# Optimization experiments

Hardware: AMD Instinct MI355X
Metric: run time of the kernel (lower is better)

Reference implementation:

```python
import jax, jax.numpy as jnp
import numpy as np

A = 2048        # atoms
IN_DEPTH = 128
OUT_DEPTH = 128
FILTER_LEN = 16


def setup_inputs() -> dict:
    key = jax.random.key(0)
    k1, k2, k3, k4 = jax.random.split(key, 4)
    node_property_tensor = jax.random.normal(k1, (A, IN_DEPTH), dtype=jnp.float32)
    connectivity_tensor = jax.random.normal(k2, (A, A, FILTER_LEN), dtype=jnp.float32)
    bond_property_tensor = jax.random.normal(k3, (A, FILTER_LEN, 2), dtype=jnp.float32)
    # filters initialized ~ N(0,1) * 1/in_depth, per the torch init
    filters = jax.random.normal(k4, (OUT_DEPTH, FILTER_LEN, IN_DEPTH + 2), dtype=jnp.float32) / IN_DEPTH
    return {
        "node_property_tensor": node_property_tensor,
        "connectivity_tensor": connectivity_tensor,
        "bond_property_tensor": bond_property_tensor,
        "filters": filters,
    }


def reference(node_property_tensor, connectivity_tensor, bond_property_tensor, filters):
    # gather neighbor features: conn (A,B,F) x node (B,D) -> (A,F,D)
    node_connection = jnp.einsum('abf,bd->afd', connectivity_tensor, node_property_tensor)
    # append bond properties -> (A, F, D+2)
    combined = jnp.concatenate([node_connection, bond_property_tensor], axis=2)
    # fused broadcast-multiply + double-sum: (A,F,K) x (O,F,K) -> (A,O)
    return jnp.einsum('afk,ofk->ao', combined, filters)
```

## Files before the change

### kernel.cpp

```cpp
#include <hip/hip_runtime.h>
#include <stdint.h>

#define N_ATOM 2048
#define K_TOT  32768
#define KCH    2048
#define BK2    128
#define NIT    (KCH / BK2)

typedef __attribute__((ext_vector_type(8))) short bf16x8;
typedef __attribute__((ext_vector_type(4))) float f32x4;

typedef __attribute__((address_space(3))) uint32_t lds_u32;
typedef __attribute__((address_space(1))) uint32_t gbl_u32;

__device__ __forceinline__ void async_ld16(const void* g, void* l) {
  __builtin_amdgcn_global_load_lds((const gbl_u32*)g, (lds_u32*)l, 16, 0, 0);
}

__device__ __forceinline__ unsigned short f2bf(float x) {
  union { float f; uint32_t u; } v; v.f = x;
  uint32_t r = v.u + 0x7FFFu + ((v.u >> 16) & 1u);
  return (unsigned short)(r >> 16);
}

__device__ __forceinline__ uint32_t pack_bf2(float x, float y) {
  union { float f; uint32_t u; } a, b;
  a.f = x; b.f = y;
  uint32_t au = a.u + 0x7FFFu;
  uint32_t bu = b.u + 0x7FFFu;
  return __builtin_amdgcn_perm(bu, au, 0x07060302u);
}

__global__ __launch_bounds__(256) void k_pre(const float* __restrict__ node,
                                             const float* __restrict__ filt,
                                             const float* __restrict__ bond,
                                             unsigned short* __restrict__ Gt,
                                             float* __restrict__ out) {
  __shared__ unsigned short SM[2 * 128 * 136];
  const int t   = threadIdx.x;
  const int bid = blockIdx.x;

  if (bid < 256) {
    unsigned short* As = SM;
    unsigned short* Bs = SM + 128 * 136;
    const int b0 = (bid & 15) * 128;
    const int n0 = (bid >> 4) * 128;

#pragma unroll
    for (int rep = 0; rep < 16; ++rep) {
      int q = rep * 256 + t;
      int row = q >> 5, c4 = q & 31;
      float4 v = *(const float4*)(node + (size_t)(b0 + row) * 128 + c4 * 4);
      unsigned short* dst = &As[row * 136 + c4 * 4];
      dst[0] = f2bf(v.x); dst[1] = f2bf(v.y); dst[2] = f2bf(v.z); dst[3] = f2bf(v.w);
    }
#pragma unroll
    for (int rep = 0; rep < 32; ++rep) {
      int q = rep * 256 + t;
      int row = q >> 6, c2 = q & 63;
      float2 v = *(const float2*)(filt + (size_t)(n0 + row) * 130 + c2 * 2);
      unsigned short* dst = &Bs[row * 136 + c2 * 2];
      dst[0] = f2bf(v.x); dst[1] = f2bf(v.y);
    }
    __syncthreads();

    const int w = t >> 6, l = t & 63;
    const int lm = l & 15, q4 = l >> 4;

    f32x4 acc[2][8];
#pragma unroll
    for (int ms = 0; ms < 2; ++ms)
#pragma unroll
      for (int ns = 0; ns < 8; ++ns)
        acc[ms][ns] = (f32x4){0.f, 0.f, 0.f, 0.f};

#pragma unroll
    for (int ks = 0; ks < 4; ++ks) {
      int ko = ks * 32 + q4 * 8;
      bf16x8 a[2], b[8];
#pragma unroll
      for (int ms = 0; ms < 2; ++ms) {
        int m = w * 32 + ms * 16 + lm;
        a[ms] = *(const bf16x8*)&As[m * 136 + ko];
      }
#pragma unroll
      for (int ns = 0; ns < 8; ++ns) {
        int n = ns * 16 + lm;
        b[ns] = *(const bf16x8*)&Bs[n * 136 + ko];
      }
#pragma unroll
      for (int ms = 0; ms < 2; ++ms)
#pragma unroll
        for (int ns = 0; ns < 8; ++ns)
          acc[ms][ns] = __builtin_amdgcn_mfma_f32_16x16x32_bf16(a[ms], b[ns], acc[ms][ns], 0, 0, 0);
    }

#pragma unroll
    for (int ms = 0; ms < 2; ++ms)
#pragma unroll
      for (int ns = 0; ns < 8; ++ns)
#pragma unroll
        for (int i = 0; i < 4; ++i) {
          int m = w * 32 + ms * 16 + q4 * 4 + i;
          int n = ns * 16 + lm;
          Gt[(size_t)(b0 + m) * 2048 + n0 + n] = f2bf(acc[ms][ns][i]);
        }
  } else {
    float* fb = (float*)SM;
    float* bl = (float*)SM + 128 * 32;
    const int a0 = (bid - 256) * 16;

#pragma unroll
    for (int r = 0; r < 16; ++r) {
      int idx = r * 256 + t;
      int o = idx >> 5, fj = idx & 31;
      int f = fj >> 1, j = fj & 1;
      fb[idx] = filt[(size_t)o * 2080 + f * 130 + 128 + j];
    }
    bl[t]       = bond[(size_t)a0 * 32 + t];
    bl[256 + t] = bond[(size_t)a0 * 32 + 256 + t];
    __syncthreads();

#pragma unroll
    for (int r = 0; r < 8; ++r) {
      int idx = r * 256 + t;
      int aa = idx >> 7, o = idx & 127;
      const float2* bp = (const float2*)&bl[aa * 32];
      const float2* fp = (const float2*)&fb[o * 32];
      float acc = 0.f;
#pragma unroll
      for (int f = 0; f < 16; ++f) {
        float2 b2 = bp[f], f2 = fp[f];
        acc += b2.x * f2.x + b2.y * f2.y;
      }
      out[(size_t)(a0 + aa) * 128 + o] = acc;
    }
  }
}

__global__ __launch_bounds__(256, 2) void k_main(const float* __restrict__ conn,
                                                 const unsigned short* __restrict__ Gt,
                                                 float* __restrict__ out) {
  __shared__ unsigned short Bh[2][8 * 128 * 16];

  const int t  = threadIdx.x;
  const int w  = t >> 6, l = t & 63;
  const int lm = l & 15, q4 = l >> 4;
  const int a0 = blockIdx.x * 64;
  const int kc = blockIdx.y * KCH;

  f32x4 acc[8];
#pragma unroll
  for (int ns = 0; ns < 8; ++ns)
    acc[ns] = (f32x4){0.f, 0.f, 0.f, 0.f};

  const float* arow = conn + (size_t)(a0 + w * 16 + lm) * K_TOT;

  auto stageB = [&](int buf, int k0) {
    const char* gB = (const char*)(Gt + (size_t)k0 * 128);
#pragma unroll
    for (int r = 0; r < 8; ++r) {
      const void* g = gB + (size_t)(r * 256 + t) * 16;
      void* lb = (void*)((char*)&Bh[buf][0] + r * 4096 + w * 1024);
      async_ld16(g, lb);
    }
  };

  f32x4 Ar[2][4][2];
#define LOADA(BUF, K0)                                                      \
  do {                                                                      \
    _Pragma("unroll") for (int kk = 0; kk < 4; ++kk) {                      \
      const float* p = arow + (K0) + kk * 32 + q4 * 8;                      \
      Ar[BUF][kk][0] = __builtin_nontemporal_load((const f32x4*)p);         \
      Ar[BUF][kk][1] = __builtin_nontemporal_load((const f32x4*)(p + 4));   \
    }                                                                       \
  } while (0)

  stageB(0, kc);
  LOADA(0, kc);
  LOADA(1, kc + BK2);
  __builtin_amdgcn_sched_barrier(0);
  asm volatile("s_waitcnt vmcnt(16)" ::: "memory");
  __builtin_amdgcn_s_barrier();
  __builtin_amdgcn_sched_barrier(0);

#pragma unroll
  for (int it = 0; it < NIT; ++it) {
    const int cur = it & 1;

    if (it + 1 < NIT) stageB(1 - cur, kc + (it + 1) * BK2);

    bf16x8 af[4];
#pragma unroll
    for (int kk = 0; kk < 4; ++kk) {
      f32x4 lo = Ar[cur][kk][0], hi = Ar[cur][kk][1];
      union { bf16x8 v; uint32_t u[4]; } cvt;
      cvt.u[0] = pack_bf2(lo[0], lo[1]);
      cvt.u[1] = pack_bf2(lo[2], lo[3]);
      cvt.u[2] = pack_bf2(hi[0], hi[1]);
      cvt.u[3] = pack_bf2(hi[2], hi[3]);
      af[kk] = cvt.v;
    }

    if (it + 2 < NIT) LOADA(cur, kc + (it + 2) * BK2);

#pragma unroll
    for (int kk = 0; kk < 4; ++kk) {
      const int b_rel = 2 * kk + (q4 >> 1);
      const int f0 = (q4 & 1) * 8;
#pragma unroll
      for (int ns = 0; ns < 8; ++ns) {
        int o = ns * 16 + lm;
        bf16x8 b = *(const bf16x8*)&Bh[cur][b_rel * 2048 + o * 16 + f0];
        acc[ns] = __builtin_amdgcn_mfma_f32_16x16x32_bf16(af[kk], b, acc[ns], 0, 0, 0);
      }
    }

    if (it + 1 < NIT) {
      __builtin_amdgcn_sched_barrier(0);
      if (it + 2 < NIT) {
        asm volatile("s_waitcnt vmcnt(8)" ::: "memory");
      } else {
        asm volatile("s_waitcnt vmcnt(0)" ::: "memory");
      }
      __builtin_amdgcn_s_barrier();
      __builtin_amdgcn_sched_barrier(0);
    }
  }
#undef LOADA

#pragma unroll
  for (int ns = 0; ns < 8; ++ns)
#pragma unroll
    for (int i = 0; i < 4; ++i) {
      int m = w * 16 + q4 * 4 + i;
      int n = ns * 16 + lm;
      atomicAdd(&out[(size_t)(a0 + m) * 128 + n], acc[ns][i]);
    }
}

extern "C" void kernel_launch(void* const* d_in, const int* in_sizes, int n_in,
                              void* d_out, int out_size, void* d_ws, size_t ws_size,
                              hipStream_t stream) {
  const float* node = (const float*)d_in[0];
  const float* conn = (const float*)d_in[1];
  const float* bond = (const float*)d_in[2];
  const float* filt = (const float*)d_in[3];
  float* out = (float*)d_out;

  if (ws_size < (size_t)N_ATOM * 2048 * sizeof(unsigned short)) return;
  unsigned short* Gt = (unsigned short*)d_ws;

  k_pre <<<dim3(384),    256, 0, stream>>>(node, filt, bond, Gt, out);
  k_main<<<dim3(32, 16), 256, 0, stream>>>(conn, Gt, out);
}
```

Baseline: 407.5 us.

## Read B operand directly from global memory instead of staging through LDS

Removes the LDS double buffer for the bf16 Gt operand in the main kernel, along with its async global-to-LDS loads, waitcnt fences and workgroup barriers. Each wave now loads its B fragments straight from global memory (expected to hit L2/L1) right before the MFMAs. This drops the barrier synchronisation and frees shared memory, which may raise occupancy. In exchange, every wave issues redundant global loads of the same B tile, and those loads now sit on the MFMA critical path with no explicit prefetch.

```diff
diff --git a/kernel.cpp b/kernel.cpp
--- a/kernel.cpp
+++ b/kernel.cpp
@@ -9,13 +9,6 @@
 
 typedef __attribute__((ext_vector_type(8))) short bf16x8;
 typedef __attribute__((ext_vector_type(4))) float f32x4;
-
-typedef __attribute__((address_space(3))) uint32_t lds_u32;
-typedef __attribute__((address_space(1))) uint32_t gbl_u32;
-
-__device__ __forceinline__ void async_ld16(const void* g, void* l) {
-  __builtin_amdgcn_global_load_lds((const gbl_u32*)g, (lds_u32*)l, 16, 0, 0);
-}
 
 __device__ __forceinline__ unsigned short f2bf(float x) {
   union { float f; uint32_t u; } v; v.f = x;
@@ -141,8 +134,6 @@
 __global__ __launch_bounds__(256, 2) void k_main(const float* __restrict__ conn,
                                                  const unsigned short* __restrict__ Gt,
                                                  float* __restrict__ out) {
-  __shared__ unsigned short Bh[2][8 * 128 * 16];
-
   const int t  = threadIdx.x;
   const int w  = t >> 6, l = t & 63;
   const int lm = l & 15, q4 = l >> 4;
@@ -156,15 +147,8 @@
 
   const float* arow = conn + (size_t)(a0 + w * 16 + lm) * K_TOT;
 
-  auto stageB = [&](int buf, int k0) {
-    const char* gB = (const char*)(Gt + (size_t)k0 * 128);
-#pragma unroll
-    for (int r = 0; r < 8; ++r) {
-      const void* g = gB + (size_t)(r * 256 + t) * 16;
-      void* lb = (void*)((char*)&Bh[buf][0] + r * 4096 + w * 1024);
-      async_ld16(g, lb);
-    }
-  };
+  const unsigned short* gB0 =
+      Gt + (size_t)(kc >> 4) * 2048 + (size_t)(q4 >> 1) * 2048 + lm * 16 + (q4 & 1) * 8;
 
   f32x4 Ar[2][4][2];
 #define LOADA(BUF, K0)                                                      \
@@ -176,19 +160,12 @@
     }                                                                       \
   } while (0)
 
-  stageB(0, kc);
   LOADA(0, kc);
   LOADA(1, kc + BK2);
-  __builtin_amdgcn_sched_barrier(0);
-  asm volatile("s_waitcnt vmcnt(16)" ::: "memory");
-  __builtin_amdgcn_s_barrier();
-  __builtin_amdgcn_sched_barrier(0);
 
 #pragma unroll
   for (int it = 0; it < NIT; ++it) {
     const int cur = it & 1;
-
-    if (it + 1 < NIT) stageB(1 - cur, kc + (it + 1) * BK2);
 
     bf16x8 af[4];
 #pragma unroll
@@ -204,27 +181,14 @@
 
     if (it + 2 < NIT) LOADA(cur, kc + (it + 2) * BK2);
 
+    const unsigned short* gB = gB0 + (size_t)it * (8 * 2048);
 #pragma unroll
     for (int kk = 0; kk < 4; ++kk) {
-      const int b_rel = 2 * kk + (q4 >> 1);
-      const int f0 = (q4 & 1) * 8;
 #pragma unroll
       for (int ns = 0; ns < 8; ++ns) {
-        int o = ns * 16 + lm;
-        bf16x8 b = *(const bf16x8*)&Bh[cur][b_rel * 2048 + o * 16 + f0];
+        bf16x8 b = *(const bf16x8*)(gB + kk * 4096 + ns * 256);
         acc[ns] = __builtin_amdgcn_mfma_f32_16x16x32_bf16(af[kk], b, acc[ns], 0, 0, 0);
       }
-    }
-
-    if (it + 1 < NIT) {
-      __builtin_amdgcn_sched_barrier(0);
-      if (it + 2 < NIT) {
-        asm volatile("s_waitcnt vmcnt(8)" ::: "memory");
-      } else {
-        asm volatile("s_waitcnt vmcnt(0)" ::: "memory");
-      }
-      __builtin_amdgcn_s_barrier();
-      __builtin_amdgcn_sched_barrier(0);
     }
   }
 #undef LOADA
```

Result: slower. 534.5 us (+31.2%).
